# Kernel tuning notes

Measured on AMD Instinct MI355X. Metric: run time of the kernel, lower is better.

The kernel has to match this reference:

```python
import jax, jax.numpy as jnp
import numpy as np

NUM_NODES = 200000
NUM_LAYERS = 3
EMBED_DIM = 64
NUM_EDGES = 3200000
NUM_PAIRS = 1000000


def setup_inputs() -> dict:
    key = jax.random.key(0)
    k1, k2, k3 = jax.random.split(key, 3)
    emb = jax.random.normal(k1, (NUM_NODES, EMBED_DIM), dtype=jnp.float32)
    alpha = jnp.ones((NUM_LAYERS + 1,), dtype=jnp.float32) * (1.0 / (NUM_LAYERS + 1))
    edge_index = jax.random.randint(k2, (2, NUM_EDGES), 0, NUM_NODES, dtype=jnp.int32)
    edge_label_index = jax.random.randint(k3, (2, NUM_PAIRS), 0, NUM_NODES, dtype=jnp.int32)
    return {"emb": emb, "alpha": alpha, "edge_index": edge_index,
            "edge_label_index": edge_label_index}


def reference(emb, alpha, edge_index, edge_label_index):
    row, col = edge_index[0], edge_index[1]  # source -> target
    # symmetric normalization (gcn_norm without self-loops, as in LGConv)
    ones = jnp.ones((row.shape[0],), dtype=emb.dtype)
    deg = jax.ops.segment_sum(ones, col, num_segments=NUM_NODES)
    dinv = jnp.where(deg > 0, jax.lax.rsqrt(jnp.maximum(deg, 1.0)), 0.0)
    norm = dinv[row] * dinv[col]  # [E]

    x = emb
    out = x * alpha[0]
    for l in range(NUM_LAYERS):
        # gather messages from sources, scale by norm, scatter-add into targets
        msgs = x[row] * norm[:, None]                      # [E, D]
        x = jax.ops.segment_sum(msgs, col, num_segments=NUM_NODES)  # [N, D]
        out = out + x * alpha[l + 1]

    src = out[edge_label_index[0]]  # [P, D]
    dst = out[edge_label_index[1]]  # [P, D]
    return jnp.sum(src * dst, axis=-1)  # [P]
```

## Files before the change

### kernel.cpp

```cpp
#include <hip/hip_runtime.h>
#include <hip/hip_fp16.h>

#define N_NODES 200000
#define N_EDGES 3200000
#define N_PAIRS 1000000
#define DIM 64
#define CAP 48
#define NPB 256
#define NB 782
#define BKTCAP 5120
#define CHUNK 16384
#define NBLK1 ((N_EDGES + CHUNK - 1) / CHUNK)

__global__ void part_kernel(const int* __restrict__ row, const int* __restrict__ col,
                            int* __restrict__ bktcnt, int* __restrict__ staging, int E) {
    __shared__ int cnt[NB];
    __shared__ int base[NB];
    for (int i = threadIdx.x; i < NB; i += 256) cnt[i] = 0;
    __syncthreads();
    int start = blockIdx.x * CHUNK;
    int end = min(start + CHUNK, E);
    for (int e = start + threadIdx.x; e < end; e += 256)
        atomicAdd(&cnt[col[e] >> 8], 1);
    __syncthreads();
    for (int i = threadIdx.x; i < NB; i += 256) {
        int c = cnt[i];
        base[i] = (c > 0) ? atomicAdd(&bktcnt[i], c) : 0;
        cnt[i] = 0;
    }
    __syncthreads();
    for (int e = start + threadIdx.x; e < end; e += 256) {
        int c = col[e];
        int r = row[e];
        int b = c >> 8;
        int off = atomicAdd(&cnt[b], 1);
        int p = base[b] + off;
        if (p < BKTCAP) staging[(size_t)b * BKTCAP + p] = ((c & 255) << 18) | r;
    }
}

__global__ void build_kernel(const int* __restrict__ staging, const int* __restrict__ bktcnt,
                             int* __restrict__ srcrow, int* __restrict__ deg,
                             float* __restrict__ dinv, int N) {
    __shared__ int tile[NPB * CAP];
    __shared__ int cur[NPB];
    int b = blockIdx.x;
    for (int i = threadIdx.x; i < NPB; i += 256) cur[i] = 0;
    __syncthreads();
    int cnt = min(bktcnt[b], BKTCAP);
    const int* st = staging + (size_t)b * BKTCAP;
    for (int i = threadIdx.x; i < cnt; i += 256) {
        int packed = st[i];
        int r = packed & 0x3FFFF;
        int cl = packed >> 18;
        int p = atomicAdd(&cur[cl], 1);
        if (p < CAP) tile[cl * CAP + p] = r;
    }
    __syncthreads();
    int nodeBase = b * NPB;
    int nvalid = min(NPB, N - nodeBase);
    for (int i = threadIdx.x; i < nvalid; i += 256) {
        int d = min(cur[i], CAP);
        deg[nodeBase + i] = d;
        dinv[nodeBase + i] = (d > 0) ? rsqrtf((float)d) : 0.0f;
    }
    int tot = nvalid * CAP;
    int* dst = srcrow + (size_t)nodeBase * CAP;
    for (int i = threadIdx.x; i < tot; i += 256) dst[i] = tile[i];
}

__global__ void convert_kernel(const float2* __restrict__ x, __half2* __restrict__ y, int n2) {
    int i = blockIdx.x * blockDim.x + threadIdx.x;
    if (i < n2) {
        float2 v = x[i];
        y[i] = __floats2half2_rn(v.x, v.y);
    }
}

__device__ __forceinline__ int rl_i(int v, int l) {
    return __builtin_amdgcn_readlane(v, l);
}
__device__ __forceinline__ float rl_f(float v, int l) {
    return __int_as_float(__builtin_amdgcn_readlane(__float_as_int(v), l));
}

__device__ __forceinline__ float gather_row(const __half* __restrict__ x, int id, float nr,
                                            int cnt, int d) {
    float acc0 = 0.0f, acc1 = 0.0f;
    int j = 0;
    for (; j + 3 < cnt; j += 4) {
        int r0 = rl_i(id, j);     float w0 = rl_f(nr, j);
        int r1 = rl_i(id, j + 1); float w1 = rl_f(nr, j + 1);
        int r2 = rl_i(id, j + 2); float w2 = rl_f(nr, j + 2);
        int r3 = rl_i(id, j + 3); float w3 = rl_f(nr, j + 3);
        float v0 = __half2float(x[(size_t)r0 * DIM + d]);
        float v1 = __half2float(x[(size_t)r1 * DIM + d]);
        float v2 = __half2float(x[(size_t)r2 * DIM + d]);
        float v3 = __half2float(x[(size_t)r3 * DIM + d]);
        acc0 += v0 * w0 + v1 * w1;
        acc1 += v2 * w2 + v3 * w3;
    }
    for (; j < cnt; ++j) {
        int r = rl_i(id, j);
        float w = rl_f(nr, j);
        acc0 += __half2float(x[(size_t)r * DIM + d]) * w;
    }
    return acc0 + acc1;
}

__global__ void prop_kernel(const __half* __restrict__ x, const int* __restrict__ srcrow,
                            const int* __restrict__ deg, const float* __restrict__ dinv,
                            __half* __restrict__ xn, int N) {
    int n = blockIdx.x * (blockDim.x >> 6) + (threadIdx.x >> 6);
    int d = threadIdx.x & 63;
    if (n >= N) return;
    int cnt = deg[n];
    int id = 0;
    float nr = 0.0f;
    if (d < cnt) {
        id = srcrow[(size_t)n * CAP + d];
        nr = dinv[id];
    }
    float acc = gather_row(x, id, nr, cnt, d);
    xn[(size_t)n * DIM + d] = __float2half(acc * dinv[n]);
}

__global__ void prop_final_kernel(const __half* __restrict__ x, const int* __restrict__ srcrow,
                                  const int* __restrict__ deg, const float* __restrict__ dinv,
                                  const __half* __restrict__ h0, const __half* __restrict__ h1,
                                  const float* __restrict__ alpha,
                                  __half* __restrict__ outh, int N) {
    int n = blockIdx.x * (blockDim.x >> 6) + (threadIdx.x >> 6);
    int d = threadIdx.x & 63;
    if (n >= N) return;
    int cnt = deg[n];
    int id = 0;
    float nr = 0.0f;
    if (d < cnt) {
        id = srcrow[(size_t)n * CAP + d];
        nr = dinv[id];
    }
    float acc = gather_row(x, id, nr, cnt, d);
    float h3 = acc * dinv[n];
    size_t o = (size_t)n * DIM + d;
    float r = alpha[0] * __half2float(h0[o]) + alpha[1] * __half2float(h1[o])
            + alpha[2] * __half2float(x[o]) + alpha[3] * h3;
    outh[o] = __float2half(r);
}

__global__ void dot_kernel(const uint2* __restrict__ outh, const int* __restrict__ pa,
                           const int* __restrict__ pb, float* __restrict__ res, int P) {
    int t = blockIdx.x * blockDim.x + threadIdx.x;
    int g = t >> 4;
    int l = threadIdx.x & 15;
    int half = P >> 1;
    if (g >= half) return;
    int p0 = g, p1 = g + half;
    int a0 = pa[p0], b0 = pb[p0];
    int a1 = pa[p1], b1 = pb[p1];
    uint2 ua0 = outh[(size_t)a0 * 16 + l];
    uint2 ub0 = outh[(size_t)b0 * 16 + l];
    uint2 ua1 = outh[(size_t)a1 * 16 + l];
    uint2 ub1 = outh[(size_t)b1 * 16 + l];
    __half2 x0 = *(__half2*)&ua0.x, x1 = *(__half2*)&ua0.y;
    __half2 y0 = *(__half2*)&ub0.x, y1 = *(__half2*)&ub0.y;
    float2 fx0 = __half22float2(x0), fx1 = __half22float2(x1);
    float2 fy0 = __half22float2(y0), fy1 = __half22float2(y1);
    float s0 = fx0.x * fy0.x + fx0.y * fy0.y + fx1.x * fy1.x + fx1.y * fy1.y;
    __half2 u0 = *(__half2*)&ua1.x, u1 = *(__half2*)&ua1.y;
    __half2 v0 = *(__half2*)&ub1.x, v1 = *(__half2*)&ub1.y;
    float2 fu0 = __half22float2(u0), fu1 = __half22float2(u1);
    float2 fv0 = __half22float2(v0), fv1 = __half22float2(v1);
    float s1 = fu0.x * fv0.x + fu0.y * fv0.y + fu1.x * fv1.x + fu1.y * fv1.y;
    s0 += __shfl_xor(s0, 1, 64);
    s1 += __shfl_xor(s1, 1, 64);
    s0 += __shfl_xor(s0, 2, 64);
    s1 += __shfl_xor(s1, 2, 64);
    s0 += __shfl_xor(s0, 4, 64);
    s1 += __shfl_xor(s1, 4, 64);
    s0 += __shfl_xor(s0, 8, 64);
    s1 += __shfl_xor(s1, 8, 64);
    if (l == 0) {
        res[p0] = s0;
        res[p1] = s1;
    }
}

extern "C" void kernel_launch(void* const* d_in, const int* in_sizes, int n_in,
                              void* d_out, int out_size, void* d_ws, size_t ws_size,
                              hipStream_t stream) {
    const float* emb   = (const float*)d_in[0];
    const float* alpha = (const float*)d_in[1];
    const int*   ei    = (const int*)d_in[2];
    const int*   eli   = (const int*)d_in[3];
    const int* row = ei;
    const int* col = ei + N_EDGES;
    const int* pa  = eli;
    const int* pb  = eli + N_PAIRS;
    float* res = (float*)d_out;

    const size_t hfeat_bytes = (size_t)N_NODES * DIM * sizeof(__half);
    char* ws = (char*)d_ws;
    size_t off = 0;
    auto alloc = [&](size_t bytes) {
        void* p = ws + off;
        off += (bytes + 255) & ~(size_t)255;
        return p;
    };
    int*    bktcnt  = (int*)alloc((size_t)NB * sizeof(int));
    int*    staging = (int*)alloc((size_t)NB * BKTCAP * sizeof(int));
    int*    srcrow  = (int*)alloc((size_t)N_NODES * CAP * sizeof(int));
    int*    deg     = (int*)alloc((size_t)N_NODES * sizeof(int));
    float*  dinv    = (float*)alloc((size_t)N_NODES * sizeof(float));
    __half* h0      = (__half*)alloc(hfeat_bytes);
    __half* h1      = (__half*)alloc(hfeat_bytes);
    __half* h2      = (__half*)alloc(hfeat_bytes);
    __half* outh    = (__half*)alloc(hfeat_bytes);

    hipMemsetAsync(bktcnt, 0, (size_t)NB * sizeof(int), stream);
    part_kernel<<<NBLK1, 256, 0, stream>>>(row, col, bktcnt, staging, N_EDGES);
    build_kernel<<<NB, 256, 0, stream>>>(staging, bktcnt, srcrow, deg, dinv, N_NODES);

    const int n2 = N_NODES * DIM / 2;
    convert_kernel<<<(n2 + 255) / 256, 256, 0, stream>>>((const float2*)emb, (__half2*)h0, n2);

    const int waves_per_block = 4;
    const int prop_grid = (N_NODES + waves_per_block - 1) / waves_per_block;
    prop_kernel<<<prop_grid, 256, 0, stream>>>(h0, srcrow, deg, dinv, h1, N_NODES);
    prop_kernel<<<prop_grid, 256, 0, stream>>>(h1, srcrow, deg, dinv, h2, N_NODES);
    prop_final_kernel<<<prop_grid, 256, 0, stream>>>(h2, srcrow, deg, dinv, h0, h1, alpha, outh, N_NODES);

    dot_kernel<<<((size_t)(N_PAIRS / 2) * 16 + 255) / 256, 256, 0, stream>>>(
        (const uint2*)outh, pa, pb, res, N_PAIRS);
}
```

Before: 438.9 us.

## Pack source degree into edge list and gather rows with 8-byte vector loads

A new pass packs each stored source id together with that source's degree into a single 32-bit word. This removes the dependent dinv[id] lookup from each propagation pass, since the weight is recomputed with rsqrt. The propagation kernels now stage (id, weight) pairs in shared memory. Each wave processes four neighbours at once, with 16 lanes loading 8-byte half4 chunks, and the partial sums are reduced with shuffles. This replaces per-lane 2-byte loads driven by readlane. The cost is an extra pass over the slot array, a block barrier, and a reliance on degree fitting in the upper 14 bits.

```diff
diff --git a/kernel.cpp b/kernel.cpp
--- a/kernel.cpp
+++ b/kernel.cpp
@@ -69,6 +69,20 @@
     for (int i = threadIdx.x; i < tot; i += 256) dst[i] = tile[i];
 }
 
+__global__ void ewpack_kernel(unsigned int* __restrict__ ew, const int* __restrict__ deg,
+                              int total) {
+    int s = blockIdx.x * blockDim.x + threadIdx.x;
+    if (s >= total) return;
+    int n = s / CAP;
+    int l = s - n * CAP;
+    unsigned int e = 0;
+    if (l < deg[n]) {
+        int r = (int)ew[s];
+        e = (unsigned int)r | ((unsigned int)deg[r] << 18);
+    }
+    ew[s] = e;
+}
+
 __global__ void convert_kernel(const float2* __restrict__ x, __half2* __restrict__ y, int n2) {
     int i = blockIdx.x * blockDim.x + threadIdx.x;
     if (i < n2) {
@@ -77,75 +91,113 @@
     }
 }
 
-__device__ __forceinline__ int rl_i(int v, int l) {
-    return __builtin_amdgcn_readlane(v, l);
-}
-__device__ __forceinline__ float rl_f(float v, int l) {
-    return __int_as_float(__builtin_amdgcn_readlane(__float_as_int(v), l));
-}
-
-__device__ __forceinline__ float gather_row(const __half* __restrict__ x, int id, float nr,
-                                            int cnt, int d) {
-    float acc0 = 0.0f, acc1 = 0.0f;
-    int j = 0;
-    for (; j + 3 < cnt; j += 4) {
-        int r0 = rl_i(id, j);     float w0 = rl_f(nr, j);
-        int r1 = rl_i(id, j + 1); float w1 = rl_f(nr, j + 1);
-        int r2 = rl_i(id, j + 2); float w2 = rl_f(nr, j + 2);
-        int r3 = rl_i(id, j + 3); float w3 = rl_f(nr, j + 3);
-        float v0 = __half2float(x[(size_t)r0 * DIM + d]);
-        float v1 = __half2float(x[(size_t)r1 * DIM + d]);
-        float v2 = __half2float(x[(size_t)r2 * DIM + d]);
-        float v3 = __half2float(x[(size_t)r3 * DIM + d]);
-        acc0 += v0 * w0 + v1 * w1;
-        acc1 += v2 * w2 + v3 * w3;
-    }
-    for (; j < cnt; ++j) {
-        int r = rl_i(id, j);
-        float w = rl_f(nr, j);
-        acc0 += __half2float(x[(size_t)r * DIM + d]) * w;
-    }
-    return acc0 + acc1;
-}
-
-__global__ void prop_kernel(const __half* __restrict__ x, const int* __restrict__ srcrow,
+__device__ __forceinline__ float2 h2f(unsigned int u) {
+    __half2 h = *(__half2*)&u;
+    return __half22float2(h);
+}
+
+__global__ void prop_kernel(const uint2* __restrict__ x, const unsigned int* __restrict__ ew,
                             const int* __restrict__ deg, const float* __restrict__ dinv,
-                            __half* __restrict__ xn, int N) {
-    int n = blockIdx.x * (blockDim.x >> 6) + (threadIdx.x >> 6);
-    int d = threadIdx.x & 63;
-    if (n >= N) return;
+                            uint2* __restrict__ xn, int N) {
+    __shared__ int2 lds[4][CAP];
+    int wv = threadIdx.x >> 6;
+    int n = blockIdx.x * 4 + wv;
+    int l = threadIdx.x & 63;
+    int q = l & 15;
+    int quarter = l >> 4;
     int cnt = deg[n];
-    int id = 0;
-    float nr = 0.0f;
-    if (d < cnt) {
-        id = srcrow[(size_t)n * CAP + d];
-        nr = dinv[id];
-    }
-    float acc = gather_row(x, id, nr, cnt, d);
-    xn[(size_t)n * DIM + d] = __float2half(acc * dinv[n]);
-}
-
-__global__ void prop_final_kernel(const __half* __restrict__ x, const int* __restrict__ srcrow,
+    if (l < CAP) {
+        unsigned int e = ew[(unsigned int)n * CAP + l];
+        int id = e & 0x3FFFF;
+        int dr = e >> 18;
+        float w = dr ? rsqrtf((float)dr) : 0.0f;
+        lds[wv][l] = make_int2(id, __float_as_int(w));
+    }
+    __syncthreads();
+    float a0 = 0.f, a1 = 0.f, a2 = 0.f, a3 = 0.f;
+    int trips = (cnt + 3) >> 2;
+    #pragma unroll 2
+    for (int k = 0; k < trips; ++k) {
+        int2 e = lds[wv][k * 4 + quarter];
+        float w = __int_as_float(e.y);
+        uint2 pix = x[(unsigned int)e.x * 16u + q];
+        float2 flo = h2f(pix.x);
+        float2 fhi = h2f(pix.y);
+        a0 += flo.x * w; a1 += flo.y * w;
+        a2 += fhi.x * w; a3 += fhi.y * w;
+    }
+    a0 += __shfl_xor(a0, 16, 64); a1 += __shfl_xor(a1, 16, 64);
+    a2 += __shfl_xor(a2, 16, 64); a3 += __shfl_xor(a3, 16, 64);
+    a0 += __shfl_xor(a0, 32, 64); a1 += __shfl_xor(a1, 32, 64);
+    a2 += __shfl_xor(a2, 32, 64); a3 += __shfl_xor(a3, 32, 64);
+    float dn = dinv[n];
+    if (quarter == 0) {
+        __half2 o01 = __floats2half2_rn(a0 * dn, a1 * dn);
+        __half2 o23 = __floats2half2_rn(a2 * dn, a3 * dn);
+        uint2 out;
+        out.x = *(unsigned int*)&o01;
+        out.y = *(unsigned int*)&o23;
+        xn[(unsigned int)n * 16u + q] = out;
+    }
+}
+
+__global__ void prop_final_kernel(const uint2* __restrict__ x, const unsigned int* __restrict__ ew,
                                   const int* __restrict__ deg, const float* __restrict__ dinv,
-                                  const __half* __restrict__ h0, const __half* __restrict__ h1,
+                                  const uint2* __restrict__ h0, const uint2* __restrict__ h1,
                                   const float* __restrict__ alpha,
-                                  __half* __restrict__ outh, int N) {
-    int n = blockIdx.x * (blockDim.x >> 6) + (threadIdx.x >> 6);
-    int d = threadIdx.x & 63;
-    if (n >= N) return;
+                                  uint2* __restrict__ outh, int N) {
+    __shared__ int2 lds[4][CAP];
+    int wv = threadIdx.x >> 6;
+    int n = blockIdx.x * 4 + wv;
+    int l = threadIdx.x & 63;
+    int q = l & 15;
+    int quarter = l >> 4;
     int cnt = deg[n];
-    int id = 0;
-    float nr = 0.0f;
-    if (d < cnt) {
-        id = srcrow[(size_t)n * CAP + d];
-        nr = dinv[id];
-    }
-    float acc = gather_row(x, id, nr, cnt, d);
-    float h3 = acc * dinv[n];
-    size_t o = (size_t)n * DIM + d;
-    float r = alpha[0] * __half2float(h0[o]) + alpha[1] * __half2float(h1[o])
-            + alpha[2] * __half2float(x[o]) + alpha[3] * h3;
-    outh[o] = __float2half(r);
+    if (l < CAP) {
+        unsigned int e = ew[(unsigned int)n * CAP + l];
+        int id = e & 0x3FFFF;
+        int dr = e >> 18;
+        float w = dr ? rsqrtf((float)dr) : 0.0f;
+        lds[wv][l] = make_int2(id, __float_as_int(w));
+    }
+    __syncthreads();
+    float a0 = 0.f, a1 = 0.f, a2 = 0.f, a3 = 0.f;
+    int trips = (cnt + 3) >> 2;
+    #pragma unroll 2
+    for (int k = 0; k < trips; ++k) {
+        int2 e = lds[wv][k * 4 + quarter];
+        float w = __int_as_float(e.y);
+        uint2 pix = x[(unsigned int)e.x * 16u + q];
+        float2 flo = h2f(pix.x);
+        float2 fhi = h2f(pix.y);
+        a0 += flo.x * w; a1 += flo.y * w;
+        a2 += fhi.x * w; a3 += fhi.y * w;
+    }
+    a0 += __shfl_xor(a0, 16, 64); a1 += __shfl_xor(a1, 16, 64);
+    a2 += __shfl_xor(a2, 16, 64); a3 += __shfl_xor(a3, 16, 64);
+    a0 += __shfl_xor(a0, 32, 64); a1 += __shfl_xor(a1, 32, 64);
+    a2 += __shfl_xor(a2, 32, 64); a3 += __shfl_xor(a3, 32, 64);
+    float dn = dinv[n];
+    if (quarter == 0) {
+        float al0 = alpha[0], al1 = alpha[1], al2 = alpha[2], al3 = alpha[3];
+        unsigned int idx = (unsigned int)n * 16u + q;
+        uint2 p0 = h0[idx];
+        uint2 p1 = h1[idx];
+        uint2 p2 = x[idx];
+        float2 f0l = h2f(p0.x), f0h = h2f(p0.y);
+        float2 f1l = h2f(p1.x), f1h = h2f(p1.y);
+        float2 f2l = h2f(p2.x), f2h = h2f(p2.y);
+        float r0 = al0 * f0l.x + al1 * f1l.x + al2 * f2l.x + al3 * (a0 * dn);
+        float r1 = al0 * f0l.y + al1 * f1l.y + al2 * f2l.y + al3 * (a1 * dn);
+        float r2 = al0 * f0h.x + al1 * f1h.x + al2 * f2h.x + al3 * (a2 * dn);
+        float r3 = al0 * f0h.y + al1 * f1h.y + al2 * f2h.y + al3 * (a3 * dn);
+        __half2 o01 = __floats2half2_rn(r0, r1);
+        __half2 o23 = __floats2half2_rn(r2, r3);
+        uint2 out;
+        out.x = *(unsigned int*)&o01;
+        out.y = *(unsigned int*)&o23;
+        outh[idx] = out;
+    }
 }
 
 __global__ void dot_kernel(const uint2* __restrict__ outh, const int* __restrict__ pa,
@@ -162,15 +214,11 @@
     uint2 ub0 = outh[(size_t)b0 * 16 + l];
     uint2 ua1 = outh[(size_t)a1 * 16 + l];
     uint2 ub1 = outh[(size_t)b1 * 16 + l];
-    __half2 x0 = *(__half2*)&ua0.x, x1 = *(__half2*)&ua0.y;
-    __half2 y0 = *(__half2*)&ub0.x, y1 = *(__half2*)&ub0.y;
-    float2 fx0 = __half22float2(x0), fx1 = __half22float2(x1);
-    float2 fy0 = __half22float2(y0), fy1 = __half22float2(y1);
+    float2 fx0 = h2f(ua0.x), fx1 = h2f(ua0.y);
+    float2 fy0 = h2f(ub0.x), fy1 = h2f(ub0.y);
     float s0 = fx0.x * fy0.x + fx0.y * fy0.y + fx1.x * fy1.x + fx1.y * fy1.y;
-    __half2 u0 = *(__half2*)&ua1.x, u1 = *(__half2*)&ua1.y;
-    __half2 v0 = *(__half2*)&ub1.x, v1 = *(__half2*)&ub1.y;
-    float2 fu0 = __half22float2(u0), fu1 = __half22float2(u1);
-    float2 fv0 = __half22float2(v0), fv1 = __half22float2(v1);
+    float2 fu0 = h2f(ua1.x), fu1 = h2f(ua1.y);
+    float2 fv0 = h2f(ub1.x), fv1 = h2f(ub1.y);
     float s1 = fu0.x * fv0.x + fu0.y * fv0.y + fu1.x * fv1.x + fu1.y * fv1.y;
     s0 += __shfl_xor(s0, 1, 64);
     s1 += __shfl_xor(s1, 1, 64);
@@ -216,19 +264,23 @@
     __half* h1      = (__half*)alloc(hfeat_bytes);
     __half* h2      = (__half*)alloc(hfeat_bytes);
     __half* outh    = (__half*)alloc(hfeat_bytes);
+    unsigned int* ew = (unsigned int*)srcrow;
 
     hipMemsetAsync(bktcnt, 0, (size_t)NB * sizeof(int), stream);
     part_kernel<<<NBLK1, 256, 0, stream>>>(row, col, bktcnt, staging, N_EDGES);
     build_kernel<<<NB, 256, 0, stream>>>(staging, bktcnt, srcrow, deg, dinv, N_NODES);
+    const int total_slots = N_NODES * CAP;
+    ewpack_kernel<<<(total_slots + 255) / 256, 256, 0, stream>>>(ew, deg, total_slots);
 
     const int n2 = N_NODES * DIM / 2;
     convert_kernel<<<(n2 + 255) / 256, 256, 0, stream>>>((const float2*)emb, (__half2*)h0, n2);
 
-    const int waves_per_block = 4;
-    const int prop_grid = (N_NODES + waves_per_block - 1) / waves_per_block;
-    prop_kernel<<<prop_grid, 256, 0, stream>>>(h0, srcrow, deg, dinv, h1, N_NODES);
-    prop_kernel<<<prop_grid, 256, 0, stream>>>(h1, srcrow, deg, dinv, h2, N_NODES);
-    prop_final_kernel<<<prop_grid, 256, 0, stream>>>(h2, srcrow, deg, dinv, h0, h1, alpha, outh, N_NODES);
+    const int prop_grid = N_NODES / 4;
+    prop_kernel<<<prop_grid, 256, 0, stream>>>((const uint2*)h0, ew, deg, dinv, (uint2*)h1, N_NODES);
+    prop_kernel<<<prop_grid, 256, 0, stream>>>((const uint2*)h1, ew, deg, dinv, (uint2*)h2, N_NODES);
+    prop_final_kernel<<<prop_grid, 256, 0, stream>>>((const uint2*)h2, ew, deg, dinv,
+                                                     (const uint2*)h0, (const uint2*)h1,
+                                                     alpha, (uint2*)outh, N_NODES);
 
     dot_kernel<<<((size_t)(N_PAIRS / 2) * 16 + 255) / 256, 256, 0, stream>>>(
         (const uint2*)outh, pa, pb, res, N_PAIRS);
```

Measured after the change: 383.7 us. -12.6%, faster.
